# Kernel tuning notes

Hardware: AMD Instinct MI355X
Metric: run time of the kernel (lower is better)

The kernel has to match this reference:

```python
import jax, jax.numpy as jnp
import numpy as np

N_NODES = 100000


def gcn_conv(x, W, b, src, dst, n):
    # PyG GCNConv: linear transform, add self-loops, symmetric deg^-1/2 norm,
    # scatter-sum messages from src -> dst, add bias.
    x = x @ W  # [N, out]
    loop = jnp.arange(n, dtype=src.dtype)
    src_sl = jnp.concatenate([src, loop])
    dst_sl = jnp.concatenate([dst, loop])
    deg = jax.ops.segment_sum(jnp.ones_like(dst_sl, dtype=x.dtype), dst_sl, num_segments=n)
    dinv = jax.lax.rsqrt(deg)
    norm = dinv[src_sl] * dinv[dst_sl]  # [E+N]
    msg = x[src_sl] * norm[:, None]
    out = jax.ops.segment_sum(msg, dst_sl, num_segments=n)
    return out + b


def base_gnn(x, edge_index, W1, b1, W2, b2):
    src, dst = edge_index[0], edge_index[1]
    n = x.shape[0]
    h = gcn_conv(x, W1, b1, src, dst, n)
    h = jax.nn.relu(h)
    return gcn_conv(h, W2, b2, src, dst, n)


def setup_inputs() -> dict:
    key = jax.random.key(0)
    ks = jax.random.split(key, 12)
    n, e, ep, en = N_NODES, 1600000, 200000, 200000
    in_ch, hid, out_ch, n_classes = 256, 128, 128, 10
    x = jax.random.normal(ks[0], (n, in_ch), dtype=jnp.float32)
    edge_index = jax.random.randint(ks[1], (2, e), 0, n, dtype=jnp.int64)
    edge_index_pos = jax.random.randint(ks[2], (2, ep), 0, n, dtype=jnp.int64)
    edge_index_neg = jax.random.randint(ks[3], (2, en), 0, n, dtype=jnp.int64)
    s1 = 1.0 / np.sqrt(in_ch)
    s2 = 1.0 / np.sqrt(hid)
    so = 1.0 / np.sqrt(out_ch)
    sl = 1.0 / np.sqrt(2 * out_ch)
    return {
        "x": x,
        "edge_index": edge_index,
        "edge_index_pos": edge_index_pos,
        "edge_index_neg": edge_index_neg,
        "W1": jax.random.uniform(ks[4], (in_ch, hid), jnp.float32, -s1, s1),
        "b1": jnp.zeros((hid,), jnp.float32),
        "W2": jax.random.uniform(ks[5], (hid, out_ch), jnp.float32, -s2, s2),
        "b2": jnp.zeros((out_ch,), jnp.float32),
        "Wcls": jax.random.uniform(ks[6], (out_ch, n_classes), jnp.float32, -so, so),
        "bcls": jax.random.uniform(ks[7], (n_classes,), jnp.float32, -so, so),
        "Wlink": jax.random.uniform(ks[8], (2 * out_ch, 1), jnp.float32, -sl, sl),
        "blink": jax.random.uniform(ks[9], (1,), jnp.float32, -sl, sl),
    }


def reference(x, edge_index, edge_index_pos, edge_index_neg,
              W1, b1, W2, b2, Wcls, bcls, Wlink, blink):
    # Shared base embedding (math identical to torch's redundant recompute)
    h = base_gnn(x, edge_index, W1, b1, W2, b2)  # [N, 128]
    # Node head
    node_logits = jax.nn.relu(h) @ Wcls + bcls
    node_pred = jax.nn.log_softmax(node_logits, axis=1)
    # Link head: gather endpoint embeddings, concat, linear
    xp = jnp.concatenate([h[edge_index_pos[0]], h[edge_index_pos[1]]], axis=1)
    xn = jnp.concatenate([h[edge_index_neg[0]], h[edge_index_neg[1]]], axis=1)
    link_pos = (xp @ Wlink + blink)[:, 0]
    link_neg = (xn @ Wlink + blink)[:, 0]
    return (node_pred, link_pos, link_neg)
```

## Files before the change

### kernel.cpp

```cpp
#include <hip/hip_runtime.h>
#include <stdint.h>

typedef __attribute__((ext_vector_type(8))) short bf16x8;
typedef __attribute__((ext_vector_type(4))) float f32x4;

__device__ __forceinline__ float b2f(uint32_t h) {
    union { uint32_t u; float f; } v; v.u = h << 16; return v.f;
}
__device__ __forceinline__ ushort f2b(float f) {
    union { float f; uint32_t u; } v; v.f = f;
    uint32_t u = v.u;
    return (ushort)((u + 0x7fffu + ((u >> 16) & 1u)) >> 16);
}
__device__ __forceinline__ float ldin(const void* p, int i, int fp32) {
    return fp32 ? ((const float*)p)[i] : b2f(((const ushort*)p)[i]);
}

__global__ void k_flags(const void* W1, const void* ei, int* flags) {
    int l = threadIdx.x;
    const ushort* w = (const ushort*)W1;
    float a0 = fabsf(b2f(w[l]));
    float a1 = fabsf(b2f(w[64 + l]));
    bool bad = !(a0 <= 0.25f) || !(a1 <= 0.25f);
    unsigned long long mb = __ballot(bad);
    const int* e = (const int*)ei;
    bool z = (l < 16) ? (e[2 * l + 1] == 0) : false;
    unsigned long long mz = __ballot(z);
    if (l == 0) {
        flags[0] = mb ? 1 : 0;
        flags[1] = (__popcll(mz & 0xffffull) >= 15) ? 1 : 0;
    }
}

__global__ __launch_bounds__(256) void k_cvt_idx(const void* ei, const void* ep, const void* en,
                                                 int* cEi, int* cEp, int* cEn,
                                                 int twoE, int twoEp, int twoEn, int N,
                                                 const int* __restrict__ flags) {
    int i = blockIdx.x * 256 + threadIdx.x;
    int i64 = flags[1];
    const void* srcp; int* dstp; int j = i;
    if (i < twoE) { srcp = ei; dstp = cEi; }
    else if (i < twoE + twoEp) { srcp = ep; dstp = cEp; j = i - twoE; }
    else if (i < twoE + twoEp + twoEn) { srcp = en; dstp = cEn; j = i - twoE - twoEp; }
    else return;
    int v = i64 ? (int)((const long long*)srcp)[j] : ((const int*)srcp)[j];
    v = v < 0 ? 0 : (v >= N ? N - 1 : v);
    dstp[j] = v;
}

__global__ __launch_bounds__(256) void k_cvt_w(const void* W1, const void* W2, const void* Wc,
                                               const void* b1, const void* b2, const void* bc,
                                               const void* Wl, const void* bl,
                                               ushort* Wt1, ushort* Wt2, ushort* WtC,
                                               ushort* b1c, ushort* b2c, ushort* bcc,
                                               ushort* Wlc, ushort* blc,
                                               const int* __restrict__ flags) {
    int i = blockIdx.x * 256 + threadIdx.x;
    int f = flags[0];
    if (i < 32768) {
        int c = i >> 8, k = i & 255;
        Wt1[i] = f2b(ldin(W1, k * 128 + c, f));
    } else if (i < 49152) {
        int j = i - 32768, c = j >> 7, k = j & 127;
        Wt2[j] = f2b(ldin(W2, k * 128 + c, f));
    } else if (i < 51200) {
        int j = i - 49152, c = j >> 7, k = j & 127;
        ushort v = 0;
        if (c < 10) v = f2b(ldin(Wc, k * 10 + c, f));
        WtC[j] = v;
    } else if (i < 51328) {
        int j = i - 51200; b1c[j] = f2b(ldin(b1, j, f));
    } else if (i < 51456) {
        int j = i - 51328; b2c[j] = f2b(ldin(b2, j, f));
    } else if (i < 51472) {
        int j = i - 51456;
        ushort v = 0;
        if (j < 10) v = f2b(ldin(bc, j, f));
        bcc[j] = v;
    } else if (i < 51728) {
        int j = i - 51472; Wlc[j] = f2b(ldin(Wl, j, f));
    } else if (i < 51736) {
        int j = i - 51728;
        ushort v = 0;
        if (j < 1) v = f2b(ldin(bl, 0, f));
        blc[j] = v;
    }
}

__global__ __launch_bounds__(256) void k_cvt_x(const void* __restrict__ x, ushort* __restrict__ xc,
                                               int total, const int* __restrict__ flags) {
    if (!flags[0]) return;
    int i = (blockIdx.x * 256 + threadIdx.x) * 8;
    if (i >= total) return;
    const float* xf = (const float*)x;
    float4 a = *(const float4*)(xf + i);
    float4 b = *(const float4*)(xf + i + 4);
    uint4 o;
    o.x = (uint32_t)f2b(a.x) | ((uint32_t)f2b(a.y) << 16);
    o.y = (uint32_t)f2b(a.z) | ((uint32_t)f2b(a.w) << 16);
    o.z = (uint32_t)f2b(b.x) | ((uint32_t)f2b(b.y) << 16);
    o.w = (uint32_t)f2b(b.z) | ((uint32_t)f2b(b.w) << 16);
    *(uint4*)(xc + i) = o;
}

__global__ __launch_bounds__(256) void k_hist1(const int* __restrict__ dst, int* __restrict__ histM,
                                               int E, int NB1) {
    __shared__ int h[512];
    for (int j = threadIdx.x; j < 512; j += 256) h[j] = 0;
    __syncthreads();
    int base = blockIdx.x * 4096;
    for (int j = threadIdx.x; j < 4096; j += 256) {
        int i = base + j;
        if (i < E) atomicAdd(&h[dst[i] >> 8], 1);
    }
    __syncthreads();
    for (int j = threadIdx.x; j < 512; j += 256)
        histM[j * NB1 + blockIdx.x] = h[j];
}

__global__ __launch_bounds__(1024) void k_mscan_block(const int* __restrict__ in, int* __restrict__ out,
                                                      int* __restrict__ bsum, int len) {
    __shared__ int sh[1024];
    int t = threadIdx.x;
    int i = blockIdx.x * 1024 + t;
    int val = (i < len) ? in[i] : 0;
    sh[t] = val; __syncthreads();
    for (int off = 1; off < 1024; off <<= 1) {
        int v = (t >= off) ? sh[t - off] : 0;
        __syncthreads();
        sh[t] += v;
        __syncthreads();
    }
    if (i < len) out[i] = sh[t] - val;
    if (t == 1023) bsum[blockIdx.x] = sh[1023];
}

__global__ __launch_bounds__(1024) void k_mscan_top(int* __restrict__ bsum, int nb) {
    __shared__ int sh[1024];
    int t = threadIdx.x;
    int val = (t < nb) ? bsum[t] : 0;
    sh[t] = val; __syncthreads();
    for (int off = 1; off < 1024; off <<= 1) {
        int v = (t >= off) ? sh[t - off] : 0;
        __syncthreads();
        sh[t] += v;
        __syncthreads();
    }
    if (t < nb) bsum[t] = sh[t] - val;
}

__global__ __launch_bounds__(1024) void k_mscan_add(int* __restrict__ out, const int* __restrict__ bsum, int len) {
    int i = blockIdx.x * 1024 + threadIdx.x;
    if (i < len) out[i] += bsum[blockIdx.x];
}

__global__ __launch_bounds__(512) void k_cbs(const int* __restrict__ off, int* __restrict__ cbs, int E, int NB1) {
    int t = threadIdx.x;
    cbs[t] = off[t * NB1];
    if (t == 0) cbs[512] = E;
}

__global__ __launch_bounds__(256) void k_scatter1(const int* __restrict__ src, const int* __restrict__ dst,
                                                  const int* __restrict__ off, int2* __restrict__ grouped,
                                                  int E, int NB1) {
    __shared__ int o[512];
    for (int j = threadIdx.x; j < 512; j += 256) o[j] = off[j * NB1 + blockIdx.x];
    __syncthreads();
    int base = blockIdx.x * 4096;
    for (int j = threadIdx.x; j < 4096; j += 256) {
        int i = base + j;
        if (i < E) {
            int d = dst[i];
            int p = atomicAdd(&o[d >> 8], 1);
            grouped[p] = make_int2(src[i], d);
        }
    }
}

__global__ __launch_bounds__(256) void k_deg2(const int2* __restrict__ grouped, const int* __restrict__ cbs,
                                              int* __restrict__ deg, int N) {
    __shared__ int c[256];
    c[threadIdx.x] = 0;
    __syncthreads();
    int b = blockIdx.x;
    int s0 = cbs[b], s1 = cbs[b + 1];
    for (int i = s0 + threadIdx.x; i < s1; i += 256)
        atomicAdd(&c[grouped[i].y & 255], 1);
    __syncthreads();
    int v = b * 256 + threadIdx.x;
    if (v < N) deg[v] = c[threadIdx.x];
}

__global__ __launch_bounds__(1024) void k_scan_block(const int* __restrict__ deg, int* __restrict__ rowptr,
                                                     float* __restrict__ dinv, int* __restrict__ bsum, int n) {
    __shared__ int sh[1024];
    int t = threadIdx.x;
    int i = blockIdx.x * 1024 + t;
    int val = (i < n) ? deg[i] : 0;
    sh[t] = val; __syncthreads();
    for (int off = 1; off < 1024; off <<= 1) {
        int v = (t >= off) ? sh[t - off] : 0;
        __syncthreads();
        sh[t] += v;
        __syncthreads();
    }
    if (i < n) {
        rowptr[i] = sh[t] - val;
        dinv[i] = rsqrtf((float)(val + 1));
    }
    if (t == 1023) bsum[blockIdx.x] = sh[1023];
}

__global__ __launch_bounds__(128) void k_scan_top(const int* __restrict__ bsum, int* __restrict__ boff, int nb) {
    __shared__ int sh[128];
    int t = threadIdx.x;
    int val = (t < nb) ? bsum[t] : 0;
    sh[t] = val; __syncthreads();
    for (int off = 1; off < 128; off <<= 1) {
        int v = (t >= off) ? sh[t - off] : 0;
        __syncthreads();
        sh[t] += v;
        __syncthreads();
    }
    if (t < nb) boff[t] = sh[t] - val;
}

__global__ __launch_bounds__(1024) void k_scan_add(int* __restrict__ rowptr, const int* __restrict__ boff,
                                                   int n, int E) {
    int i = blockIdx.x * 1024 + threadIdx.x;
    if (i < n) rowptr[i] += boff[blockIdx.x];
    if (i == 0) rowptr[n] = E;
}

__global__ __launch_bounds__(256) void k_fill2(const int2* __restrict__ grouped, const int* __restrict__ cbs,
                                               const int* __restrict__ rowptr, const float* __restrict__ dinv,
                                               int2* __restrict__ edge, int N) {
    __shared__ int o[256];
    int b = blockIdx.x;
    int v = b * 256 + threadIdx.x;
    o[threadIdx.x] = (v < N) ? rowptr[v] : 0;
    __syncthreads();
    int s0 = cbs[b], s1 = cbs[b + 1];
    for (int i = s0 + threadIdx.x; i < s1; i += 256) {
        int2 e = grouped[i];
        int p = atomicAdd(&o[e.y & 255], 1);
        float w = dinv[e.x] * dinv[e.y];
        edge[p] = make_int2(e.x, __float_as_int(w));
    }
}

template <int K, bool SEL>
__global__ __launch_bounds__(256, 2) void k_gemm(const void* __restrict__ Xraw,
                                                 const ushort* __restrict__ Xc,
                                                 const int* __restrict__ flags,
                                                 const ushort* __restrict__ Wt,
                                                 ushort* __restrict__ Out, int nrows) {
    constexpr int NS = K / 32;
    __shared__ uint4 sB[NS * 8 * 64];

    const int tid = threadIdx.x;
    for (int it = tid; it < NS * 8 * 64; it += 256) {
        int l = it & 63, fn = it >> 6;
        int s = fn >> 3, n = fn & 7;
        int mr = l & 15, q = l >> 4;
        sB[it] = *(const uint4*)(Wt + (size_t)(n * 16 + mr) * K + s * 32 + q * 8);
    }
    __syncthreads();

    const ushort* Xp = SEL ? (flags[0] ? Xc : (const ushort*)Xraw) : (const ushort*)Xraw;
    const int wave = tid >> 6;
    const int l = tid & 63;
    const int q = l >> 4, mr = l & 15;
    const int gw = blockIdx.x * 4 + wave;
    const int nw = gridDim.x * 4;
    const int ntile = (nrows + 15) >> 4;

    for (int tp = gw; tp * 2 < ntile; tp += nw) {
        const int t0 = tp * 2;
        const bool has1 = (t0 + 1 < ntile);
        const int t1 = has1 ? t0 + 1 : t0;
        const int r0 = min(t0 * 16 + mr, nrows - 1);
        const int r1 = min(t1 * 16 + mr, nrows - 1);

        bf16x8 a0[NS], a1[NS];
        const ushort* x0 = Xp + (size_t)r0 * K + q * 8;
        const ushort* x1 = Xp + (size_t)r1 * K + q * 8;
#pragma unroll
        for (int s = 0; s < NS; ++s) a0[s] = *(const bf16x8*)(x0 + s * 32);
#pragma unroll
        for (int s = 0; s < NS; ++s) a1[s] = *(const bf16x8*)(x1 + s * 32);

        f32x4 acc0[8], acc1[8];
#pragma unroll
        for (int n = 0; n < 8; ++n) {
            acc0[n] = (f32x4){0.f, 0.f, 0.f, 0.f};
            acc1[n] = (f32x4){0.f, 0.f, 0.f, 0.f};
        }
#pragma unroll
        for (int s = 0; s < NS; ++s) {
#pragma unroll
            for (int n = 0; n < 8; ++n) {
                bf16x8 b = __builtin_bit_cast(bf16x8, sB[(s * 8 + n) * 64 + l]);
                acc0[n] = __builtin_amdgcn_mfma_f32_16x16x32_bf16(a0[s], b, acc0[n], 0, 0, 0);
                acc1[n] = __builtin_amdgcn_mfma_f32_16x16x32_bf16(a1[s], b, acc1[n], 0, 0, 0);
            }
        }
#pragma unroll
        for (int n = 0; n < 8; ++n) {
#pragma unroll
            for (int r = 0; r < 4; ++r) {
                int row0 = t0 * 16 + q * 4 + r;
                if (row0 < nrows) Out[(size_t)row0 * 128 + n * 16 + mr] = f2b(acc0[n][r]);
                if (has1) {
                    int row1 = t1 * 16 + q * 4 + r;
                    if (row1 < nrows) Out[(size_t)row1 * 128 + n * 16 + mr] = f2b(acc1[n][r]);
                }
            }
        }
    }
}

__global__ __launch_bounds__(256) void k_conv(const ushort* __restrict__ XW, const int* __restrict__ rowptr,
                                              const int2* __restrict__ edge, const float* __restrict__ dinv,
                                              const ushort* __restrict__ bias, ushort* __restrict__ Hout,
                                              int n, int relu) {
    int wave = threadIdx.x >> 6;
    int v = blockIdx.x * 4 + wave;
    if (v >= n) return;
    int l = threadIdx.x & 63;

    int s0 = rowptr[v], s1 = rowptr[v + 1];
    float dv = dinv[v];
    uint32_t pv = *(const uint32_t*)(XW + (size_t)v * 128 + 2 * l);
    float wself = dv * dv;
    float acc0 = b2f(pv & 0xffffu) * wself;
    float acc1 = b2f(pv >> 16) * wself;

    int i = s0;
    while (i + 8 <= s1) {
        int2 e0[8];
#pragma unroll
        for (int j = 0; j < 8; ++j) e0[j] = edge[i + j];
        uint32_t p[8];
#pragma unroll
        for (int j = 0; j < 8; ++j)
            p[j] = *(const uint32_t*)(XW + (size_t)e0[j].x * 128 + 2 * l);
#pragma unroll
        for (int j = 0; j < 8; ++j) {
            float w = __int_as_float(e0[j].y);
            acc0 += b2f(p[j] & 0xffffu) * w;
            acc1 += b2f(p[j] >> 16) * w;
        }
        i += 8;
    }
    if (i < s1) {
        int2 e0[8];
#pragma unroll
        for (int j = 0; j < 8; ++j) e0[j] = edge[(i + j < s1) ? (i + j) : s0];
        uint32_t p[8];
#pragma unroll
        for (int j = 0; j < 8; ++j)
            p[j] = *(const uint32_t*)(XW + (size_t)e0[j].x * 128 + 2 * l);
#pragma unroll
        for (int j = 0; j < 8; ++j) {
            float w = (i + j < s1) ? __int_as_float(e0[j].y) : 0.f;
            acc0 += b2f(p[j] & 0xffffu) * w;
            acc1 += b2f(p[j] >> 16) * w;
        }
    }

    uint32_t bb = *(const uint32_t*)(bias + 2 * l);
    acc0 += b2f(bb & 0xffffu);
    acc1 += b2f(bb >> 16);
    if (relu) { acc0 = fmaxf(acc0, 0.f); acc1 = fmaxf(acc1, 0.f); }

    uint32_t o = (uint32_t)f2b(acc0) | ((uint32_t)f2b(acc1) << 16);
    *(uint32_t*)(Hout + (size_t)v * 128 + 2 * l) = o;
}

__global__ __launch_bounds__(256) void k_nodehead(const ushort* __restrict__ H, const ushort* __restrict__ WtC,
                                                  const ushort* __restrict__ bcc, void* __restrict__ out,
                                                  int n, const int* __restrict__ flags) {
    int wave = threadIdx.x >> 6;
    int gw = blockIdx.x * 4 + wave;
    if (gw * 16 >= n) return;
    int fp32o = flags[0];
    int l = threadIdx.x & 63;
    int q = l >> 4, mr = l & 15;
    int m0 = gw * 16;

    f32x4 acc = (f32x4){0.f, 0.f, 0.f, 0.f};
    const ushort* hrow = H + (size_t)(m0 + mr) * 128 + q * 8;
#pragma unroll
    for (int s = 0; s < 4; ++s) {
        bf16x8 a = *(const bf16x8*)(hrow + s * 32);
#pragma unroll
        for (int j = 0; j < 8; ++j) {
            ushort t = (ushort)a[j];
            if (t & 0x8000u) a[j] = 0;
        }
        bf16x8 b = *(const bf16x8*)(WtC + (size_t)mr * 128 + s * 32 + q * 8);
        acc = __builtin_amdgcn_mfma_f32_16x16x32_bf16(a, b, acc, 0, 0, 0);
    }

    float bc = b2f(bcc[mr]);
#pragma unroll
    for (int r = 0; r < 4; ++r) {
        float logit = acc[r] + bc;
        float m = (mr < 10) ? logit : -1e30f;
#pragma unroll
        for (int off = 1; off < 16; off <<= 1) m = fmaxf(m, __shfl_xor(m, off, 16));
        float ex = (mr < 10) ? expf(logit - m) : 0.f;
        float ssum = ex;
#pragma unroll
        for (int off = 1; off < 16; off <<= 1) ssum += __shfl_xor(ssum, off, 16);
        if (mr < 10) {
            float lsm = logit - m - logf(ssum);
            size_t idx = (size_t)(m0 + q * 4 + r) * 10 + mr;
            if (fp32o) ((float*)out)[idx] = lsm;
            else ((ushort*)out)[idx] = f2b(lsm);
        }
    }
}

__global__ __launch_bounds__(256) void k_link(const ushort* __restrict__ H, const int* __restrict__ pos,
                                              const int* __restrict__ neg, const ushort* __restrict__ Wlc,
                                              const ushort* __restrict__ blc, void* __restrict__ out,
                                              size_t obase, int Ep, int En, const int* __restrict__ flags) {
    int wave = threadIdx.x >> 6;
    int l = threadIdx.x & 63;
    int g = l >> 4, t = l & 15;
    int e = (blockIdx.x * 4 + wave) * 4 + g;
    if (e >= Ep + En) return;
    int fp32o = flags[0];

    const int* P; int eb, off2;
    if (e < Ep) { P = pos; eb = e; off2 = Ep; }
    else { P = neg; eb = e - Ep; off2 = En; }
    int sI = P[eb], dI = P[off2 + eb];

    bf16x8 hs = *(const bf16x8*)(H + (size_t)sI * 128 + t * 8);
    bf16x8 hd = *(const bf16x8*)(H + (size_t)dI * 128 + t * 8);
    bf16x8 w0 = *(const bf16x8*)(Wlc + t * 8);
    bf16x8 w1 = *(const bf16x8*)(Wlc + 128 + t * 8);

    float acc = 0.f;
#pragma unroll
    for (int j = 0; j < 8; ++j) {
        acc += b2f((ushort)hs[j]) * b2f((ushort)w0[j]);
        acc += b2f((ushort)hd[j]) * b2f((ushort)w1[j]);
    }
#pragma unroll
    for (int off = 1; off < 16; off <<= 1) acc += __shfl_xor(acc, off, 16);
    if (t == 0) {
        float vf = acc + b2f(blc[0]);
        size_t idx = obase + (size_t)e;
        if (fp32o) ((float*)out)[idx] = vf;
        else ((ushort*)out)[idx] = f2b(vf);
    }
}

extern "C" void kernel_launch(void* const* d_in, const int* in_sizes, int n_in,
                              void* d_out, int out_size, void* d_ws, size_t ws_size,
                              hipStream_t stream) {
    const void* x    = d_in[0];
    const void* ei   = d_in[1];
    const void* eip  = d_in[2];
    const void* ein  = d_in[3];
    const void* W1   = d_in[4];
    const void* b1   = d_in[5];
    const void* W2   = d_in[6];
    const void* b2   = d_in[7];
    const void* Wcls = d_in[8];
    const void* bcls = d_in[9];
    const void* Wl   = d_in[10];
    const void* bl   = d_in[11];

    const int N  = in_sizes[0] / 256;
    const int E  = in_sizes[1] / 2;
    const int Ep = in_sizes[2] / 2;
    const int En = in_sizes[3] / 2;

    const int NB1  = (E + 4095) / 4096;
    const int mlen = 512 * NB1;
    const int mb   = (mlen + 1023) / 1024;

    char* ws = (char*)d_ws;
    size_t off = 0;
    auto alloc = [&](size_t bytes) -> void* {
        void* p = ws + off;
        off = (off + bytes + 255) & ~(size_t)255;
        return p;
    };
    int*    flags  = (int*)alloc(256);
    ushort* xc     = (ushort*)alloc((size_t)N * 256 * 2);
    ushort* bufXW  = (ushort*)alloc((size_t)N * 128 * 2);
    ushort* bufH   = (ushort*)alloc((size_t)N * 128 * 2);
    int*    cEi    = (int*)alloc((size_t)2 * E * 4);
    int*    cEp    = (int*)alloc((size_t)2 * Ep * 4);
    int*    cEn    = (int*)alloc((size_t)2 * En * 4);
    int2*   grouped= (int2*)alloc((size_t)E * 8);
    int*    histM  = (int*)alloc((size_t)mlen * 4);
    int*    offM   = (int*)alloc((size_t)mlen * 4);
    int*    msum   = (int*)alloc(4096);
    int*    cbs    = (int*)alloc(513 * 4);
    float*  dinv   = (float*)alloc((size_t)N * 4);
    int*    deg    = (int*)alloc((size_t)N * 4);
    int*    rowp   = (int*)alloc((size_t)(N + 1) * 4);
    int2*   edge   = (int2*)alloc((size_t)E * 8);
    int*    bsum   = (int*)alloc(1024);
    int*    boff   = (int*)alloc(1024);
    ushort* Wt1    = (ushort*)alloc(65536);
    ushort* Wt2    = (ushort*)alloc(32768);
    ushort* WtC    = (ushort*)alloc(4096);
    ushort* b1c    = (ushort*)alloc(256);
    ushort* b2c    = (ushort*)alloc(256);
    ushort* bcc    = (ushort*)alloc(64);
    ushort* Wlc    = (ushort*)alloc(512);
    ushort* blc    = (ushort*)alloc(64);

    k_flags<<<1, 64, 0, stream>>>(W1, ei, flags);

    int twoE = 2 * E, twoEp = 2 * Ep, twoEn = 2 * En;
    int idx_total = twoE + twoEp + twoEn;
    k_cvt_idx<<<(idx_total + 255) / 256, 256, 0, stream>>>(ei, eip, ein, cEi, cEp, cEn,
                                                           twoE, twoEp, twoEn, N, flags);
    k_cvt_w<<<203, 256, 0, stream>>>(W1, W2, Wcls, b1, b2, bcls, Wl, bl,
                                     Wt1, Wt2, WtC, b1c, b2c, bcc, Wlc, blc, flags);
    k_cvt_x<<<((N * 256 / 8) + 255) / 256, 256, 0, stream>>>(x, xc, N * 256, flags);

    const int* srcp = cEi;
    const int* dstp = cEi + E;

    k_hist1<<<NB1, 256, 0, stream>>>(dstp, histM, E, NB1);
    k_mscan_block<<<mb, 1024, 0, stream>>>(histM, offM, msum, mlen);
    k_mscan_top<<<1, 1024, 0, stream>>>(msum, mb);
    k_mscan_add<<<mb, 1024, 0, stream>>>(offM, msum, mlen);
    k_cbs<<<1, 512, 0, stream>>>(offM, cbs, E, NB1);
    k_scatter1<<<NB1, 256, 0, stream>>>(srcp, dstp, offM, grouped, E, NB1);
    k_deg2<<<512, 256, 0, stream>>>(grouped, cbs, deg, N);
    int nb = (N + 1023) / 1024;
    k_scan_block<<<nb, 1024, 0, stream>>>(deg, rowp, dinv, bsum, N);
    k_scan_top<<<1, 128, 0, stream>>>(bsum, boff, nb);
    k_scan_add<<<nb, 1024, 0, stream>>>(rowp, boff, N, E);
    k_fill2<<<512, 256, 0, stream>>>(grouped, cbs, rowp, dinv, edge, N);

    k_gemm<256, true><<<512, 256, 0, stream>>>(x, xc, flags, Wt1, bufXW, N);
    k_conv<<<(N + 3) / 4, 256, 0, stream>>>(bufXW, rowp, edge, dinv, b1c, bufH, N, 1);
    k_gemm<128, false><<<768, 256, 0, stream>>>(bufH, bufH, flags, Wt2, bufXW, N);
    k_conv<<<(N + 3) / 4, 256, 0, stream>>>(bufXW, rowp, edge, dinv, b2c, bufH, N, 0);

    int head_blocks = ((N + 15) / 16 + 3) / 4;
    k_nodehead<<<head_blocks, 256, 0, stream>>>(bufH, WtC, bcc, d_out, N, flags);
    k_link<<<(Ep + En + 3) / 4, 256, 0, stream>>>(bufH, cEp, cEn, Wlc, blc, d_out,
                                                  (size_t)N * 10, Ep, En, flags);
}
```

Baseline: 527.4 us.

## Fuse fp32 to bf16 input conversion into GEMM and widen conv gathers

Drops the separate x conversion kernel and its bf16 staging buffer. The first GEMM now loads fp32 rows and packs them to bf16 in registers, which removes one full write and one full read of the converted input. The aggregation kernel is also restructured so each lane gathers 16-byte chunks, with four edges processed in parallel per wave. The four partial sums are then combined with cross-lane shuffles. The trade-offs are higher register pressure in the GEMM and fewer in-flight gathers per lane in the conv.

```diff
diff --git a/kernel.cpp b/kernel.cpp
--- a/kernel.cpp
+++ b/kernel.cpp
@@ -14,6 +14,14 @@
 }
 __device__ __forceinline__ float ldin(const void* p, int i, int fp32) {
     return fp32 ? ((const float*)p)[i] : b2f(((const ushort*)p)[i]);
+}
+__device__ __forceinline__ bf16x8 pack8(float4 a, float4 b) {
+    bf16x8 r;
+    r[0] = (short)f2b(a.x); r[1] = (short)f2b(a.y);
+    r[2] = (short)f2b(a.z); r[3] = (short)f2b(a.w);
+    r[4] = (short)f2b(b.x); r[5] = (short)f2b(b.y);
+    r[6] = (short)f2b(b.z); r[7] = (short)f2b(b.w);
+    return r;
 }
 
 __global__ void k_flags(const void* W1, const void* ei, int* flags) {
@@ -87,22 +95,6 @@
     }
 }
 
-__global__ __launch_bounds__(256) void k_cvt_x(const void* __restrict__ x, ushort* __restrict__ xc,
-                                               int total, const int* __restrict__ flags) {
-    if (!flags[0]) return;
-    int i = (blockIdx.x * 256 + threadIdx.x) * 8;
-    if (i >= total) return;
-    const float* xf = (const float*)x;
-    float4 a = *(const float4*)(xf + i);
-    float4 b = *(const float4*)(xf + i + 4);
-    uint4 o;
-    o.x = (uint32_t)f2b(a.x) | ((uint32_t)f2b(a.y) << 16);
-    o.y = (uint32_t)f2b(a.z) | ((uint32_t)f2b(a.w) << 16);
-    o.z = (uint32_t)f2b(b.x) | ((uint32_t)f2b(b.y) << 16);
-    o.w = (uint32_t)f2b(b.z) | ((uint32_t)f2b(b.w) << 16);
-    *(uint4*)(xc + i) = o;
-}
-
 __global__ __launch_bounds__(256) void k_hist1(const int* __restrict__ dst, int* __restrict__ histM,
                                                int E, int NB1) {
     __shared__ int h[512];
@@ -251,7 +243,6 @@
 
 template <int K, bool SEL>
 __global__ __launch_bounds__(256, 2) void k_gemm(const void* __restrict__ Xraw,
-                                                 const ushort* __restrict__ Xc,
                                                  const int* __restrict__ flags,
                                                  const ushort* __restrict__ Wt,
                                                  ushort* __restrict__ Out, int nrows) {
@@ -267,7 +258,7 @@
     }
     __syncthreads();
 
-    const ushort* Xp = SEL ? (flags[0] ? Xc : (const ushort*)Xraw) : (const ushort*)Xraw;
+    const bool f32in = SEL && flags[0];
     const int wave = tid >> 6;
     const int l = tid & 63;
     const int q = l >> 4, mr = l & 15;
@@ -283,12 +274,29 @@
         const int r1 = min(t1 * 16 + mr, nrows - 1);
 
         bf16x8 a0[NS], a1[NS];
-        const ushort* x0 = Xp + (size_t)r0 * K + q * 8;
-        const ushort* x1 = Xp + (size_t)r1 * K + q * 8;
-#pragma unroll
-        for (int s = 0; s < NS; ++s) a0[s] = *(const bf16x8*)(x0 + s * 32);
-#pragma unroll
-        for (int s = 0; s < NS; ++s) a1[s] = *(const bf16x8*)(x1 + s * 32);
+        if (f32in) {
+            const float* x0 = (const float*)Xraw + (size_t)r0 * K + q * 8;
+            const float* x1 = (const float*)Xraw + (size_t)r1 * K + q * 8;
+#pragma unroll
+            for (int s = 0; s < NS; ++s) {
+                float4 a = *(const float4*)(x0 + s * 32);
+                float4 b = *(const float4*)(x0 + s * 32 + 4);
+                a0[s] = pack8(a, b);
+            }
+#pragma unroll
+            for (int s = 0; s < NS; ++s) {
+                float4 a = *(const float4*)(x1 + s * 32);
+                float4 b = *(const float4*)(x1 + s * 32 + 4);
+                a1[s] = pack8(a, b);
+            }
+        } else {
+            const ushort* x0 = (const ushort*)Xraw + (size_t)r0 * K + q * 8;
+            const ushort* x1 = (const ushort*)Xraw + (size_t)r1 * K + q * 8;
+#pragma unroll
+            for (int s = 0; s < NS; ++s) a0[s] = *(const bf16x8*)(x0 + s * 32);
+#pragma unroll
+            for (int s = 0; s < NS; ++s) a1[s] = *(const bf16x8*)(x1 + s * 32);
+        }
 
         f32x4 acc0[8], acc1[8];
 #pragma unroll
@@ -320,6 +328,17 @@
     }
 }
 
+__device__ __forceinline__ void fma8(float* acc, uint4 p, float w) {
+    uint32_t pu[4] = {p.x, p.y, p.z, p.w};
+#pragma unroll
+    for (int k = 0; k < 4; ++k) {
+        float lo = __uint_as_float(pu[k] << 16);
+        float hi = __uint_as_float(pu[k] & 0xffff0000u);
+        acc[2 * k]     += lo * w;
+        acc[2 * k + 1] += hi * w;
+    }
+}
+
 __global__ __launch_bounds__(256) void k_conv(const ushort* __restrict__ XW, const int* __restrict__ rowptr,
                                               const int2* __restrict__ edge, const float* __restrict__ dinv,
                                               const ushort* __restrict__ bias, ushort* __restrict__ Hout,
@@ -328,54 +347,68 @@
     int v = blockIdx.x * 4 + wave;
     if (v >= n) return;
     int l = threadIdx.x & 63;
+    int g = l >> 4;
+    int c = l & 15;
 
     int s0 = rowptr[v], s1 = rowptr[v + 1];
     float dv = dinv[v];
-    uint32_t pv = *(const uint32_t*)(XW + (size_t)v * 128 + 2 * l);
-    float wself = dv * dv;
-    float acc0 = b2f(pv & 0xffffu) * wself;
-    float acc1 = b2f(pv >> 16) * wself;
+    float wself = (g == 0) ? dv * dv : 0.f;
+
+    uint4 pv = *(const uint4*)(XW + (size_t)v * 128 + c * 8);
+    float acc[8];
+    {
+        uint32_t pu[4] = {pv.x, pv.y, pv.z, pv.w};
+#pragma unroll
+        for (int k = 0; k < 4; ++k) {
+            acc[2 * k]     = __uint_as_float(pu[k] << 16) * wself;
+            acc[2 * k + 1] = __uint_as_float(pu[k] & 0xffff0000u) * wself;
+        }
+    }
 
     int i = s0;
     while (i + 8 <= s1) {
-        int2 e0[8];
-#pragma unroll
-        for (int j = 0; j < 8; ++j) e0[j] = edge[i + j];
-        uint32_t p[8];
-#pragma unroll
-        for (int j = 0; j < 8; ++j)
-            p[j] = *(const uint32_t*)(XW + (size_t)e0[j].x * 128 + 2 * l);
-#pragma unroll
-        for (int j = 0; j < 8; ++j) {
-            float w = __int_as_float(e0[j].y);
-            acc0 += b2f(p[j] & 0xffffu) * w;
-            acc1 += b2f(p[j] >> 16) * w;
-        }
+        int2 eA = edge[i + g];
+        int2 eB = edge[i + 4 + g];
+        uint4 pA = *(const uint4*)(XW + (size_t)eA.x * 128 + c * 8);
+        uint4 pB = *(const uint4*)(XW + (size_t)eB.x * 128 + c * 8);
+        fma8(acc, pA, __int_as_float(eA.y));
+        fma8(acc, pB, __int_as_float(eB.y));
         i += 8;
     }
+    if (i + 4 <= s1) {
+        int2 e = edge[i + g];
+        uint4 p = *(const uint4*)(XW + (size_t)e.x * 128 + c * 8);
+        fma8(acc, p, __int_as_float(e.y));
+        i += 4;
+    }
     if (i < s1) {
-        int2 e0[8];
-#pragma unroll
-        for (int j = 0; j < 8; ++j) e0[j] = edge[(i + j < s1) ? (i + j) : s0];
-        uint32_t p[8];
-#pragma unroll
-        for (int j = 0; j < 8; ++j)
-            p[j] = *(const uint32_t*)(XW + (size_t)e0[j].x * 128 + 2 * l);
-#pragma unroll
-        for (int j = 0; j < 8; ++j) {
-            float w = (i + j < s1) ? __int_as_float(e0[j].y) : 0.f;
-            acc0 += b2f(p[j] & 0xffffu) * w;
-            acc1 += b2f(p[j] >> 16) * w;
-        }
-    }
-
-    uint32_t bb = *(const uint32_t*)(bias + 2 * l);
-    acc0 += b2f(bb & 0xffffu);
-    acc1 += b2f(bb >> 16);
-    if (relu) { acc0 = fmaxf(acc0, 0.f); acc1 = fmaxf(acc1, 0.f); }
-
-    uint32_t o = (uint32_t)f2b(acc0) | ((uint32_t)f2b(acc1) << 16);
-    *(uint32_t*)(Hout + (size_t)v * 128 + 2 * l) = o;
+        int ei = i + g;
+        bool val = ei < s1;
+        int2 e = edge[val ? ei : s0];
+        uint4 p = *(const uint4*)(XW + (size_t)e.x * 128 + c * 8);
+        fma8(acc, p, val ? __int_as_float(e.y) : 0.f);
+    }
+
+#pragma unroll
+    for (int k = 0; k < 8; ++k) {
+        acc[k] += __shfl_xor(acc[k], 16);
+        acc[k] += __shfl_xor(acc[k], 32);
+    }
+
+    if (g == 0) {
+        uint4 bb = *(const uint4*)(bias + c * 8);
+        uint32_t bu[4] = {bb.x, bb.y, bb.z, bb.w};
+        uint4 o;
+        uint32_t* op = (uint32_t*)&o;
+#pragma unroll
+        for (int k = 0; k < 4; ++k) {
+            float lo = acc[2 * k]     + __uint_as_float(bu[k] << 16);
+            float hi = acc[2 * k + 1] + __uint_as_float(bu[k] & 0xffff0000u);
+            if (relu) { lo = fmaxf(lo, 0.f); hi = fmaxf(hi, 0.f); }
+            op[k] = (uint32_t)f2b(lo) | ((uint32_t)f2b(hi) << 16);
+        }
+        *(uint4*)(Hout + (size_t)v * 128 + c * 8) = o;
+    }
 }
 
 __global__ __launch_bounds__(256) void k_nodehead(const ushort* __restrict__ H, const ushort* __restrict__ WtC,
@@ -493,7 +526,6 @@
         return p;
     };
     int*    flags  = (int*)alloc(256);
-    ushort* xc     = (ushort*)alloc((size_t)N * 256 * 2);
     ushort* bufXW  = (ushort*)alloc((size_t)N * 128 * 2);
     ushort* bufH   = (ushort*)alloc((size_t)N * 128 * 2);
     int*    cEi    = (int*)alloc((size_t)2 * E * 4);
@@ -527,7 +559,6 @@
                                                            twoE, twoEp, twoEn, N, flags);
     k_cvt_w<<<203, 256, 0, stream>>>(W1, W2, Wcls, b1, b2, bcls, Wl, bl,
                                      Wt1, Wt2, WtC, b1c, b2c, bcc, Wlc, blc, flags);
-    k_cvt_x<<<((N * 256 / 8) + 255) / 256, 256, 0, stream>>>(x, xc, N * 256, flags);
 
     const int* srcp = cEi;
     const int* dstp = cEi + E;
@@ -545,9 +576,9 @@
     k_scan_add<<<nb, 1024, 0, stream>>>(rowp, boff, N, E);
     k_fill2<<<512, 256, 0, stream>>>(grouped, cbs, rowp, dinv, edge, N);
 
-    k_gemm<256, true><<<512, 256, 0, stream>>>(x, xc, flags, Wt1, bufXW, N);
+    k_gemm<256, true><<<512, 256, 0, stream>>>(x, flags, Wt1, bufXW, N);
     k_conv<<<(N + 3) / 4, 256, 0, stream>>>(bufXW, rowp, edge, dinv, b1c, bufH, N, 1);
-    k_gemm<128, false><<<768, 256, 0, stream>>>(bufH, bufH, flags, Wt2, bufXW, N);
+    k_gemm<128, false><<<768, 256, 0, stream>>>(bufH, flags, Wt2, bufXW, N);
     k_conv<<<(N + 3) / 4, 256, 0, stream>>>(bufXW, rowp, edge, dinv, b2c, bufH, N, 0);
 
     int head_blocks = ((N + 15) / 16 + 3) / 4;
```

Result: no change. 525.0 us (-0.4%).
